# Kernel tuning notes

Hardware: AMD Instinct MI355X
Metric: run time of the kernel (lower is better)

Reference implementation:

```python
import jax, jax.numpy as jnp
import numpy as np

TAPS_INT = [-12, -34, -56, -42, 18, 120, 260, 380, 400, 290, 60, -210, -430, -500,
            -380, -120, 180, 430, 540, 480, 280, 20, -220, -370, -400, -310, -150,
            10, 120, 160, 130, 60]
SCALE = 65536  # power-of-two fixed-point scale -> floor(acc/SCALE) is exact in fp32
L = len(TAPS_INT)  # 32 taps
N = 16777216       # 2^24 samples


def setup_inputs() -> dict:
    key = jax.random.key(0)
    # integer-valued samples; |x| < ~1000 keeps all intermediate sums exactly
    # representable in float32 (< 2^24), so this matches the int64 torch math.
    x = jnp.round(jax.random.normal(key, (N,), dtype=jnp.float32) * 170.0)
    taps = jnp.asarray(TAPS_INT, dtype=jnp.float32)
    return {"x": x, "taps": taps}


def reference(x, taps):
    n_len = x.shape[0]
    xi = jnp.trunc(x)  # x.to(torch.int64) truncates toward zero (no-op here: x integral)
    # causal FIR: acc[n] = sum_k x[n-k] * taps[k]  == full convolution, first N samples
    acc = jnp.convolve(xi, taps, mode='full')[:n_len]
    y = jnp.floor(acc / SCALE)  # acc // scale (floor division), exact: SCALE = 2^16
    n = jnp.arange(n_len)
    # original loop runs for n in [L, N); y[0:L] stays zero
    return jnp.where(n >= L, y, 0.0).astype(jnp.float32)
```

## Files before the change

### kernel.cpp

```cpp
#include <hip/hip_runtime.h>
#include <math.h>

__device__ __constant__ const float TAPS[32] = {
    -12.f,  -34.f,  -56.f,  -42.f,   18.f,  120.f,  260.f,  380.f,
    400.f,  290.f,   60.f, -210.f, -430.f, -500.f, -380.f, -120.f,
    180.f,  430.f,  540.f,  480.f,  280.f,   20.f, -220.f, -370.f,
   -400.f, -310.f, -150.f,   10.f,  120.f,  160.f,  130.f,   60.f
};

#define SCALE_INV (1.0f / 65536.0f)
#define TILE 4096
#define HALO 32
#define NF4_IN ((TILE + HALO) / 4)
#define NF4_OUT (TILE / 4)

__device__ __forceinline__ int swz(int q) { return q ^ ((q >> 3) & 7); }

__global__ __launch_bounds__(256)
void fir32_lds(const float* __restrict__ x, float* __restrict__ y, int n) {
    __shared__ float4 s_in[NF4_IN];
    __shared__ float4 s_out[NF4_OUT];

    const int tid = threadIdx.x;
    const long tile = (long)blockIdx.x * TILE;
    const long base4 = (tile - HALO) / 4;
    const long n4 = n >> 2;

    const float4* x4 = reinterpret_cast<const float4*>(x);
    #pragma unroll
    for (int v = 0; v < 5; ++v) {
        int f = v * 256 + tid;
        if (f < NF4_IN) {
            long i4 = base4 + f;
            float4 val = make_float4(0.f, 0.f, 0.f, 0.f);
            if (i4 >= 0 && i4 < n4) val = x4[i4];
            s_in[swz(f)] = val;
        }
    }
    __syncthreads();

    float w[48];
    #pragma unroll
    for (int v = 0; v < 12; ++v) {
        int q = 4 * tid + v;
        float4 t = s_in[swz(q)];
        w[4 * v + 0] = t.x;
        w[4 * v + 1] = t.y;
        w[4 * v + 2] = t.z;
        w[4 * v + 3] = t.w;
    }

    const bool head = (blockIdx.x == 0 && tid < 2);
    float acc[16];
    #pragma unroll
    for (int j = 0; j < 16; ++j) {
        float a = 0.0f;
        #pragma unroll
        for (int k = 0; k < 32; ++k) {
            a = fmaf(w[32 + j - k], TAPS[k], a);
        }
        float r = floorf(a * SCALE_INV);
        acc[j] = head ? 0.0f : r;
    }

    #pragma unroll
    for (int v = 0; v < 4; ++v) {
        int q = 4 * tid + v;
        s_out[swz(q)] = make_float4(acc[4 * v + 0], acc[4 * v + 1],
                                    acc[4 * v + 2], acc[4 * v + 3]);
    }
    __syncthreads();

    float4* y4 = reinterpret_cast<float4*>(y) + (tile >> 2);
    #pragma unroll
    for (int v = 0; v < 4; ++v) {
        int f = v * 256 + tid;
        if (tile + 4L * f < n) y4[f] = s_out[swz(f)];
    }
}

extern "C" void kernel_launch(void* const* d_in, const int* in_sizes, int n_in,
                              void* d_out, int out_size, void* d_ws, size_t ws_size,
                              hipStream_t stream) {
    const float* x = (const float*)d_in[0];
    float* y = (float*)d_out;
    const int n = in_sizes[0];

    const int grid = (int)(((long)n + TILE - 1) / TILE);
    fir32_lds<<<dim3(grid), dim3(256), 0, stream>>>(x, y, n);
}
```

Before: 29.41 us.

## Use 4 outputs per thread with direct float4 stores and no output staging

Each thread now computes 4 consecutive outputs instead of 16, with a 2048-sample tile, 512 threads per block and a plain LDS input layout without swizzle. The LDS output staging buffer and second barrier are dropped, so each thread writes its float4 straight to global memory with coalesced addresses. This lowers register pressure and raises parallelism. In exchange the 32-sample halo is loaded and read by more threads, so each thread reloads 36 inputs to produce only 4 outputs.

```diff
diff --git a/kernel.cpp b/kernel.cpp
--- a/kernel.cpp
+++ b/kernel.cpp
@@ -9,73 +9,62 @@
 };
 
 #define SCALE_INV (1.0f / 65536.0f)
-#define TILE 4096
+#define TILE 2048
 #define HALO 32
-#define NF4_IN ((TILE + HALO) / 4)
-#define NF4_OUT (TILE / 4)
+#define NT   512
+#define NF4  ((TILE + HALO) / 4)
 
-__device__ __forceinline__ int swz(int q) { return q ^ ((q >> 3) & 7); }
-
-__global__ __launch_bounds__(256)
-void fir32_lds(const float* __restrict__ x, float* __restrict__ y, int n) {
-    __shared__ float4 s_in[NF4_IN];
-    __shared__ float4 s_out[NF4_OUT];
+__global__ __launch_bounds__(NT)
+void fir32_lds4(const float* __restrict__ x, float* __restrict__ y, int n) {
+    __shared__ float4 s_in[NF4];
 
     const int tid = threadIdx.x;
-    const long tile = (long)blockIdx.x * TILE;
-    const long base4 = (tile - HALO) / 4;
-    const long n4 = n >> 2;
+    const long tile4 = (long)blockIdx.x * (TILE / 4);
+    const long base4 = tile4 - (HALO / 4);
+    const long n4 = (long)n >> 2;
+    const float4* x4 = reinterpret_cast<const float4*>(x);
 
-    const float4* x4 = reinterpret_cast<const float4*>(x);
-    #pragma unroll
-    for (int v = 0; v < 5; ++v) {
-        int f = v * 256 + tid;
-        if (f < NF4_IN) {
-            long i4 = base4 + f;
-            float4 val = make_float4(0.f, 0.f, 0.f, 0.f);
-            if (i4 >= 0 && i4 < n4) val = x4[i4];
-            s_in[swz(f)] = val;
+    {
+        long g0 = base4 + tid;
+        float4 v = make_float4(0.f, 0.f, 0.f, 0.f);
+        if (g0 >= 0 && g0 < n4) v = x4[g0];
+        s_in[tid] = v;
+        if (tid < NF4 - NT) {
+            long g1 = g0 + NT;
+            float4 h = make_float4(0.f, 0.f, 0.f, 0.f);
+            if (g1 >= 0 && g1 < n4) h = x4[g1];
+            s_in[tid + NT] = h;
         }
     }
     __syncthreads();
 
-    float w[48];
+    float w[36];
     #pragma unroll
-    for (int v = 0; v < 12; ++v) {
-        int q = 4 * tid + v;
-        float4 t = s_in[swz(q)];
-        w[4 * v + 0] = t.x;
-        w[4 * v + 1] = t.y;
-        w[4 * v + 2] = t.z;
-        w[4 * v + 3] = t.w;
+    for (int j = 0; j < 9; ++j) {
+        float4 t = s_in[tid + j];
+        w[4 * j + 0] = t.x;
+        w[4 * j + 1] = t.y;
+        w[4 * j + 2] = t.z;
+        w[4 * j + 3] = t.w;
     }
 
-    const bool head = (blockIdx.x == 0 && tid < 2);
-    float acc[16];
+    const bool zero_head = (blockIdx.x == 0) && (tid < 8);
+
+    float acc[4];
     #pragma unroll
-    for (int j = 0; j < 16; ++j) {
+    for (int j = 0; j < 4; ++j) {
         float a = 0.0f;
         #pragma unroll
         for (int k = 0; k < 32; ++k) {
             a = fmaf(w[32 + j - k], TAPS[k], a);
         }
-        float r = floorf(a * SCALE_INV);
-        acc[j] = head ? 0.0f : r;
+        acc[j] = zero_head ? 0.0f : floorf(a * SCALE_INV);
     }
 
-    #pragma unroll
-    for (int v = 0; v < 4; ++v) {
-        int q = 4 * tid + v;
-        s_out[swz(q)] = make_float4(acc[4 * v + 0], acc[4 * v + 1],
-                                    acc[4 * v + 2], acc[4 * v + 3]);
-    }
-    __syncthreads();
-
-    float4* y4 = reinterpret_cast<float4*>(y) + (tile >> 2);
-    #pragma unroll
-    for (int v = 0; v < 4; ++v) {
-        int f = v * 256 + tid;
-        if (tile + 4L * f < n) y4[f] = s_out[swz(f)];
+    const long o = tile4 + tid;
+    if (o < n4) {
+        reinterpret_cast<float4*>(y)[o] =
+            make_float4(acc[0], acc[1], acc[2], acc[3]);
     }
 }
 
@@ -87,5 +76,5 @@
     const int n = in_sizes[0];
 
     const int grid = (int)(((long)n + TILE - 1) / TILE);
-    fir32_lds<<<dim3(grid), dim3(256), 0, stream>>>(x, y, n);
+    fir32_lds4<<<dim3(grid), dim3(NT), 0, stream>>>(x, y, n);
 }
```

Result: slower. 41.81 us (+42.1%).
